# Kernel tuning notes

Measured on AMD Instinct MI355X. Metric: run time of the kernel, lower is better.

## Reference

```python
import jax, jax.numpy as jnp
from jax import lax
import numpy as np

COST_CLASS = 1.0
COST_BEZIER = 5.0
INF = jnp.float32(1e30)


def setup_inputs() -> dict:
    key = jax.random.key(0)
    k1, k2, k3, k4 = jax.random.split(key, 4)
    B, N, M, C = 16, 256, 256, 4096
    return {
        'pred_ctrl': jax.random.normal(k1, (B, N, 4, 2), dtype=jnp.float32),
        'pred_logits': jax.random.normal(k2, (B, N, C), dtype=jnp.float32),
        'gt_ctrl': jax.random.normal(k3, (B, M, 4, 2), dtype=jnp.float32),
        'gt_labels': jax.random.randint(k4, (B, M), 0, C, dtype=jnp.int64),
    }


def build_cost(pred_ctrl, pred_logits, gt_ctrl, gt_labels):
    B, N = pred_ctrl.shape[:2]
    M = gt_ctrl.shape[1]
    prob = jax.nn.softmax(pred_logits, axis=-1)                      # (B,N,C)
    lbl = jnp.broadcast_to(gt_labels[:, None, :], (B, N, M))          # (B,N,M)
    cost_class = -jnp.take_along_axis(prob, lbl, axis=2)              # (B,N,M)
    p = pred_ctrl.reshape(B, N, 8)
    g = gt_ctrl.reshape(B, M, 8)
    cost_bezier = jnp.sum(jnp.abs(p[:, :, None, :] - g[:, None, :, :]), axis=-1)  # L1 cdist
    return COST_CLASS * cost_class + COST_BEZIER * cost_bezier        # (B,N,M)


def lsa(cost):
    """Jonker-Volgenant shortest augmenting path, square n x n cost.
    Returns (row_ind, col_ind) matching scipy.optimize.linear_sum_assignment."""
    n = cost.shape[0]
    ar = jnp.arange(n)

    def solve_row(carry, cur_row):
        u, v, row4col, col4row = carry

        def cond(s):
            return s['sink'] < 0

        def body(s):
            i = s['i']
            SR = s['SR'].at[i].set(True)
            r = s['minVal'] + cost[i] - u[i] - v
            better = (r < s['spc']) & (~s['SC'])
            path = jnp.where(better, i, s['path'])
            spc = jnp.where(better, r, s['spc'])
            masked = jnp.where(s['SC'], INF, spc)
            j = jnp.argmin(masked).astype(jnp.int32)
            minVal = masked[j]
            SC = s['SC'].at[j].set(True)
            hit_free = row4col[j] < 0
            sink = jnp.where(hit_free, j, jnp.int32(-1))
            i_next = jnp.where(hit_free, i, row4col[j])
            return dict(i=i_next, minVal=minVal, SR=SR, SC=SC, spc=spc, path=path, sink=sink)

        init = dict(i=cur_row.astype(jnp.int32), minVal=jnp.float32(0),
                    SR=jnp.zeros(n, bool), SC=jnp.zeros(n, bool),
                    spc=jnp.full(n, INF), path=jnp.full(n, -1, jnp.int32),
                    sink=jnp.int32(-1))
        s = lax.while_loop(cond, body, init)
        minVal, SR, SC, spc, path, sink = s['minVal'], s['SR'], s['SC'], s['spc'], s['path'], s['sink']

        # dual updates
        u = u.at[cur_row].add(minVal)
        safe = jnp.clip(col4row, 0, n - 1)
        u = jnp.where(SR & (ar != cur_row), u + minVal - spc[safe], u)
        v = jnp.where(SC, v - (minVal - spc), v)

        # augment along predecessor path
        def aug_cond(t):
            return ~t['done']

        def aug_body(t):
            j = t['j']
            i = path[j]
            r4c = t['row4col'].at[j].set(i)
            j_next = t['col4row'][i]
            c4r = t['col4row'].at[i].set(j)
            return dict(j=j_next, row4col=r4c, col4row=c4r, done=(i == cur_row))

        t = lax.while_loop(aug_cond, aug_body,
                           dict(j=sink, row4col=row4col, col4row=col4row, done=jnp.bool_(False)))
        return (u, v, t['row4col'], t['col4row']), None

    init = (jnp.zeros(n, jnp.float32), jnp.zeros(n, jnp.float32),
            jnp.full(n, -1, jnp.int32), jnp.full(n, -1, jnp.int32))
    (u, v, row4col, col4row), _ = lax.scan(solve_row, init, ar)
    return ar.astype(jnp.int64), col4row.astype(jnp.int64)


_batched_lsa = jax.jit(jax.vmap(lsa))


def reference(pred_ctrl, pred_logits, gt_ctrl, gt_labels):
    C = build_cost(pred_ctrl, pred_logits, gt_ctrl, gt_labels)  # (B,N,M)
    row_ind, col_ind = _batched_lsa(C)                           # each (B,N)
    return row_ind, col_ind, C
```

## Files before the change

kernel.cpp:

```cpp
#include <hip/hip_runtime.h>

#define BATCH 16
#define NROW  256
#define MCOL  256
#define CDIM  4096
#define INF_F 1e30f
#define CROWS 150
#define MAXSWEEP 32
#define FREETHRESH 6

__global__ __launch_bounds__(256)
void cost_fused_kernel(const float* __restrict__ pred_ctrl,
                       const float* __restrict__ logits,
                       const float* __restrict__ gt_ctrl,
                       const int* __restrict__ gt_labels,
                       float* __restrict__ Cout) {
    const int bn = blockIdx.x;
    const int b  = bn >> 8;
    const int t  = threadIdx.x;
    const int lane = t & 63, wave = t >> 6;
    const float* rp = logits + (size_t)bn * CDIM;

    __shared__ float part[4];
    __shared__ float smax, ssum;

    float mx = -INF_F;
    for (int c = t; c < CDIM; c += 256) mx = fmaxf(mx, rp[c]);
    for (int off = 32; off; off >>= 1) mx = fmaxf(mx, __shfl_down(mx, off));
    if (lane == 0) part[wave] = mx;
    __syncthreads();
    if (t == 0) smax = fmaxf(fmaxf(part[0], part[1]), fmaxf(part[2], part[3]));
    __syncthreads();
    mx = smax;

    float s = 0.f;
    for (int c = t; c < CDIM; c += 256) s += expf(rp[c] - mx);
    for (int off = 32; off; off >>= 1) s += __shfl_down(s, off);
    __syncthreads();
    if (lane == 0) part[wave] = s;
    __syncthreads();
    if (t == 0) ssum = part[0] + part[1] + part[2] + part[3];
    __syncthreads();

    const float rmax = smax, rsum = ssum;
    const int m = t;

    const float* pp = pred_ctrl + (size_t)bn * 8;
    const float p0 = pp[0], p1 = pp[1], p2 = pp[2], p3 = pp[3];
    const float p4 = pp[4], p5 = pp[5], p6 = pp[6], p7 = pp[7];

    const float* gp = gt_ctrl + ((size_t)b * MCOL + m) * 8;
    const float4 ga = *(const float4*)gp;
    const float4 gb = *(const float4*)(gp + 4);

    const int lbl = gt_labels[b * MCOL + m];
    const float prob = expf(rp[lbl] - rmax) / rsum;

    float cb = fabsf(p0 - ga.x);
    cb += fabsf(p1 - ga.y);
    cb += fabsf(p2 - ga.z);
    cb += fabsf(p3 - ga.w);
    cb += fabsf(p4 - gb.x);
    cb += fabsf(p5 - gb.y);
    cb += fabsf(p6 - gb.z);
    cb += fabsf(p7 - gb.w);

    Cout[(size_t)bn * MCOL + m] = -prob + 5.0f * cb;
}

__device__ __forceinline__ unsigned ordkey(float f) {
    unsigned b = __float_as_uint(f);
    return (b & 0x80000000u) ? ~b : (b | 0x80000000u);
}
__device__ __forceinline__ float unordkey(unsigned k) {
    unsigned b = (k & 0x80000000u) ? (k ^ 0x80000000u) : ~k;
    return __uint_as_float(b);
}

template<int CTRL>
__device__ __forceinline__ unsigned dpp_min_step(unsigned x) {
    const unsigned o = (unsigned)__builtin_amdgcn_update_dpp((int)x, (int)x, CTRL, 0xf, 0xf, false);
    return o < x ? o : x;
}
__device__ __forceinline__ unsigned wave_min_u32(unsigned x) {
    x = dpp_min_step<0x111>(x);
    x = dpp_min_step<0x112>(x);
    x = dpp_min_step<0x114>(x);
    x = dpp_min_step<0x118>(x);
    x = dpp_min_step<0x142>(x);
    x = dpp_min_step<0x143>(x);
    return (unsigned)__builtin_amdgcn_readlane((int)x, 63);
}

__device__ __forceinline__ float readlane_f(float x, int lane_idx) {
    return __int_as_float(__builtin_amdgcn_readlane(__float_as_int(x), lane_idx));
}
__device__ __forceinline__ float sel4f(float a0, float a1, float a2, float a3, int s) {
    float r = a0;
    r = (s == 1) ? a1 : r;
    r = (s == 2) ? a2 : r;
    r = (s == 3) ? a3 : r;
    return r;
}
__device__ __forceinline__ int sel4i(int a0, int a1, int a2, int a3, int s) {
    int r = a0;
    r = (s == 1) ? a1 : r;
    r = (s == 2) ? a2 : r;
    r = (s == 3) ? a3 : r;
    return r;
}

__global__ __launch_bounds__(64)
void lsa_kernel(const float* __restrict__ Cmat,
                float* __restrict__ out_row,
                float* __restrict__ out_col) {
    const int b = blockIdx.x;
    const int t = threadIdx.x;
    const int jb = 4 * t;
    const float* C = Cmat + (size_t)b * NROW * MCOL;

    __shared__ float Cc[CROWS][MCOL];
    __shared__ __align__(16) float v_lds[MCOL];
    __shared__ unsigned long long bid_s[MCOL];
    __shared__ int r4c_s[MCOL];
    __shared__ int c4r_s[NROW];
    int* const argrow_s = (int*)bid_s;

    float m0 = INF_F, m1 = INF_F, m2 = INF_F, m3 = INF_F;
    int   r0 = 0, r1 = 0, r2 = 0, r3 = 0;
    for (int i = 0; i < NROW; i++) {
        const float4 c4 = *(const float4*)(C + (size_t)i * MCOL + jb);
        if (i < CROWS) *(float4*)&Cc[i][jb] = c4;
        if (c4.x < m0) { m0 = c4.x; r0 = i; }
        if (c4.y < m1) { m1 = c4.y; r1 = i; }
        if (c4.z < m2) { m2 = c4.z; r2 = i; }
        if (c4.w < m3) { m3 = c4.w; r3 = i; }
    }
    float u0 = 0.f, u1 = 0.f, u2 = 0.f, u3 = 0.f;

    v_lds[jb + 0] = m0; v_lds[jb + 1] = m1;
    v_lds[jb + 2] = m2; v_lds[jb + 3] = m3;
    argrow_s[jb + 0] = r0; argrow_s[jb + 1] = r1;
    argrow_s[jb + 2] = r2; argrow_s[jb + 3] = r3;
    for (int k = 0; k < 4; k++) { c4r_s[jb + k] = -1; r4c_s[jb + k] = -1; }
    __syncthreads();

    if (t == 0) {
        for (int j = 0; j < MCOL; j++) {
            const int r = argrow_s[j];
            if (c4r_s[r] < 0) { c4r_s[r] = j; r4c_s[j] = r; }
        }
    }
    __syncthreads();

    for (int sweep = 0; sweep < MAXSWEEP; sweep++) {
        const int4 myc = *(const int4*)&c4r_s[jb];
        const unsigned long long f0 = __ballot(myc.x < 0);
        const unsigned long long f1 = __ballot(myc.y < 0);
        const unsigned long long f2 = __ballot(myc.z < 0);
        const unsigned long long f3 = __ballot(myc.w < 0);
        const int nfree = __popcll(f0) + __popcll(f1) + __popcll(f2) + __popcll(f3);
        if (nfree <= FREETHRESH) break;

        bid_s[jb + 0] = 0; bid_s[jb + 1] = 0;
        bid_s[jb + 2] = 0; bid_s[jb + 3] = 0;
        __syncthreads();

        const bool fr[4] = { myc.x < 0, myc.y < 0, myc.z < 0, myc.w < 0 };
        int bj[4]; float gap[4], mu2v[4]; unsigned long long key[4];

        #pragma unroll
        for (int s = 0; s < 4; s++) {
            bj[s] = -1; gap[s] = 0.f; mu2v[s] = 0.f; key[s] = 0;
            if (!fr[s]) continue;
            const int i = jb + s;
            const float* rowp = C + (size_t)i * MCOL;
            unsigned bk1 = 0xFFFFFFFFu, bk2 = 0xFFFFFFFFu; int bjj = 0;
            for (int j = 0; j < MCOL; j += 4) {
                const float4 vv = *(const float4*)&v_lds[j];
                const float4 cc = *(const float4*)(rowp + j);
                unsigned k;
                k = ordkey(cc.x - vv.x); if (k < bk1) { bk2 = bk1; bk1 = k; bjj = j + 0; } else if (k < bk2) bk2 = k;
                k = ordkey(cc.y - vv.y); if (k < bk1) { bk2 = bk1; bk1 = k; bjj = j + 1; } else if (k < bk2) bk2 = k;
                k = ordkey(cc.z - vv.z); if (k < bk1) { bk2 = bk1; bk1 = k; bjj = j + 2; } else if (k < bk2) bk2 = k;
                k = ordkey(cc.w - vv.w); if (k < bk1) { bk2 = bk1; bk1 = k; bjj = j + 3; } else if (k < bk2) bk2 = k;
            }
            const float mu1 = unordkey(bk1), mu2 = unordkey(bk2);
            gap[s] = mu2 - mu1; mu2v[s] = mu2; bj[s] = bjj;
            key[s] = ((unsigned long long)ordkey(gap[s]) << 32) | (unsigned)i;
            atomicMax(&bid_s[bjj], key[s]);
        }
        __syncthreads();

        int kold[4];
        #pragma unroll
        for (int s = 0; s < 4; s++) {
            kold[s] = -2;
            if (bj[s] >= 0 && bid_s[bj[s]] == key[s]) kold[s] = r4c_s[bj[s]];
        }
        __syncthreads();

        #pragma unroll
        for (int s = 0; s < 4; s++) {
            if (kold[s] >= -1) {
                const int i = jb + s, j1 = bj[s];
                r4c_s[j1] = i;
                c4r_s[i] = j1;
                if (kold[s] >= 0) c4r_s[kold[s]] = -1;
                v_lds[j1] -= gap[s];
                if (s == 0) u0 = mu2v[0];
                else if (s == 1) u1 = mu2v[1];
                else if (s == 2) u2 = mu2v[2];
                else u3 = mu2v[3];
            }
        }
        __syncthreads();
    }

    int4 q;
    q = *(const int4*)&r4c_s[jb];
    int rc0 = q.x, rc1 = q.y, rc2 = q.z, rc3 = q.w;
    q = *(const int4*)&c4r_s[jb];
    int cr0 = q.x, cr1 = q.y, cr2 = q.z, cr3 = q.w;
    const float4 vq = *(const float4*)&v_lds[jb];
    float v0 = vq.x, v1 = vq.y, v2 = vq.z, v3 = vq.w;

    unsigned long long mm0 = __ballot(cr0 < 0);
    unsigned long long mm1 = __ballot(cr1 < 0);
    unsigned long long mm2 = __ballot(cr2 < 0);
    unsigned long long mm3 = __ballot(cr3 < 0);

    while (mm0 | mm1 | mm2 | mm3) {
        int cur;
        if      (mm0) { const int l = __ffsll(mm0) - 1; mm0 &= mm0 - 1; cur = 4 * l + 0; }
        else if (mm1) { const int l = __ffsll(mm1) - 1; mm1 &= mm1 - 1; cur = 4 * l + 1; }
        else if (mm2) { const int l = __ffsll(mm2) - 1; mm2 &= mm2 - 1; cur = 4 * l + 2; }
        else          { const int l = __ffsll(mm3) - 1; mm3 &= mm3 - 1; cur = 4 * l + 3; }

        float s0 = INF_F, s1 = INF_F, s2 = INF_F, s3 = INF_F;
        int   p0 = -1,    p1 = -1,    p2 = -1,    p3 = -1;
        float e0 = 0.f, e1 = 0.f, e2 = 0.f, e3 = 0.f;
        int scmask = 0, srmask = 0;
        int i = cur, sink = -1;
        float minVal = 0.f;

        for (int it = 0; it < MCOL; it++) {
            if ((i >> 2) == t) {
                const int s = i & 3;
                srmask |= 1 << s;
                e0 = s == 0 ? minVal : e0; e1 = s == 1 ? minVal : e1;
                e2 = s == 2 ? minVal : e2; e3 = s == 3 ? minVal : e3;
            }
            const float ui = readlane_f(sel4f(u0, u1, u2, u3, i & 3), i >> 2);
            float4 c4;
            if (i < CROWS) c4 = *(const float4*)&Cc[i][jb];
            else           c4 = *(const float4*)(C + (size_t)i * MCOL + jb);
            const float base = minVal - ui;
            float d;
            d = base + c4.x - v0; if (!(scmask & 1) && d < s0) { s0 = d; p0 = i; }
            d = base + c4.y - v1; if (!(scmask & 2) && d < s1) { s1 = d; p1 = i; }
            d = base + c4.z - v2; if (!(scmask & 4) && d < s2) { s2 = d; p2 = i; }
            d = base + c4.w - v3; if (!(scmask & 8) && d < s3) { s3 = d; p3 = i; }

            unsigned lmin = 0xFFFFFFFFu; int lslot = 0, lrc = -1;
            if (!(scmask & 1)) { const unsigned k = ordkey(s0); if (k < lmin) { lmin = k; lslot = 0; lrc = rc0; } }
            if (!(scmask & 2)) { const unsigned k = ordkey(s1); if (k < lmin) { lmin = k; lslot = 1; lrc = rc1; } }
            if (!(scmask & 4)) { const unsigned k = ordkey(s2); if (k < lmin) { lmin = k; lslot = 2; lrc = rc2; } }
            if (!(scmask & 8)) { const unsigned k = ordkey(s3); if (k < lmin) { lmin = k; lslot = 3; lrc = rc3; } }

            const unsigned g = wave_min_u32(lmin);
            const unsigned long long bal = __ballot(lmin == g);
            const int w = __ffsll(bal) - 1;
            const int pk = __builtin_amdgcn_readlane(((lrc + 1) << 2) | lslot, w);
            const int mj = 4 * w + (pk & 3);
            const int rcx = (pk >> 2) - 1;
            minVal = unordkey(g);

            if (w == t) scmask |= 1 << (pk & 3);
            if (rcx < 0) { sink = mj; break; }
            i = rcx;
        }

        if (srmask & 1) u0 += minVal - e0;
        if (srmask & 2) u1 += minVal - e1;
        if (srmask & 4) u2 += minVal - e2;
        if (srmask & 8) u3 += minVal - e3;
        if (scmask & 1) v0 -= (minVal - s0);
        if (scmask & 2) v1 -= (minVal - s1);
        if (scmask & 4) v2 -= (minVal - s2);
        if (scmask & 8) v3 -= (minVal - s3);

        int j = sink;
        for (int g2 = 0; g2 < NROW; g2++) {
            const int pi = __builtin_amdgcn_readlane(
                sel4i(p0, p1, p2, p3, j & 3), j >> 2);
            if ((j >> 2) == t) {
                const int s = j & 3;
                rc0 = s == 0 ? pi : rc0; rc1 = s == 1 ? pi : rc1;
                rc2 = s == 2 ? pi : rc2; rc3 = s == 3 ? pi : rc3;
            }
            const int jn = __builtin_amdgcn_readlane(
                sel4i(cr0, cr1, cr2, cr3, pi & 3), pi >> 2);
            if ((pi >> 2) == t) {
                const int s = pi & 3;
                cr0 = s == 0 ? j : cr0; cr1 = s == 1 ? j : cr1;
                cr2 = s == 2 ? j : cr2; cr3 = s == 3 ? j : cr3;
            }
            if (jn < 0) break;
            j = jn;
        }
    }

    out_row[b * NROW + jb + 0] = (float)(jb + 0);
    out_row[b * NROW + jb + 1] = (float)(jb + 1);
    out_row[b * NROW + jb + 2] = (float)(jb + 2);
    out_row[b * NROW + jb + 3] = (float)(jb + 3);
    out_col[b * NROW + jb + 0] = (float)cr0;
    out_col[b * NROW + jb + 1] = (float)cr1;
    out_col[b * NROW + jb + 2] = (float)cr2;
    out_col[b * NROW + jb + 3] = (float)cr3;
}

extern "C" void kernel_launch(void* const* d_in, const int* in_sizes, int n_in,
                              void* d_out, int out_size, void* d_ws, size_t ws_size,
                              hipStream_t stream) {
    const float* pred_ctrl   = (const float*)d_in[0];
    const float* pred_logits = (const float*)d_in[1];
    const float* gt_ctrl     = (const float*)d_in[2];
    const int*   gt_labels   = (const int*)d_in[3];

    float* out     = (float*)d_out;
    float* out_row = out;
    float* out_col = out + BATCH * NROW;
    float* Cout    = out + 2 * BATCH * NROW;

    cost_fused_kernel<<<BATCH * NROW, 256, 0, stream>>>(pred_ctrl, pred_logits,
                                                        gt_ctrl, gt_labels, Cout);
    lsa_kernel<<<BATCH, 64, 0, stream>>>(Cout, out_row, out_col);
}
```

Before: 1.784 ms.

## Replace greedy init and auction sweeps with epsilon-scaled auction warm start

Drops the column-min greedy initial assignment and the gap-based sweep loop that stopped at a small free-row threshold. In their place it runs an epsilon-scaling auction: four eps levels, the assignment is reset at each level, with per-level and total sweep caps. Afterwards it recomputes row duals as reduced-cost minima and unassigns any rows whose current match is not tight, so the exact augmenting-path phase starts from feasible duals. The aim is fewer rows left for the serial shortest-path augmentation. The risk is more auction sweeps, and possibly more rows unassigned by the tightness check.

```diff
diff --git a/kernel.cpp b/kernel.cpp
--- a/kernel.cpp
+++ b/kernel.cpp
@@ -6,8 +6,9 @@
 #define CDIM  4096
 #define INF_F 1e30f
 #define CROWS 150
-#define MAXSWEEP 32
-#define FREETHRESH 6
+#define NSCALE 4
+#define SWEEPCAP 40
+#define TOTBUDGET 120
 
 __global__ __launch_bounds__(256)
 void cost_fused_kernel(const float* __restrict__ pred_ctrl,
@@ -124,98 +125,113 @@
     __shared__ unsigned long long bid_s[MCOL];
     __shared__ int r4c_s[MCOL];
     __shared__ int c4r_s[NROW];
-    int* const argrow_s = (int*)bid_s;
 
     float m0 = INF_F, m1 = INF_F, m2 = INF_F, m3 = INF_F;
-    int   r0 = 0, r1 = 0, r2 = 0, r3 = 0;
     for (int i = 0; i < NROW; i++) {
         const float4 c4 = *(const float4*)(C + (size_t)i * MCOL + jb);
         if (i < CROWS) *(float4*)&Cc[i][jb] = c4;
-        if (c4.x < m0) { m0 = c4.x; r0 = i; }
-        if (c4.y < m1) { m1 = c4.y; r1 = i; }
-        if (c4.z < m2) { m2 = c4.z; r2 = i; }
-        if (c4.w < m3) { m3 = c4.w; r3 = i; }
+        m0 = fminf(m0, c4.x); m1 = fminf(m1, c4.y);
+        m2 = fminf(m2, c4.z); m3 = fminf(m3, c4.w);
     }
     float u0 = 0.f, u1 = 0.f, u2 = 0.f, u3 = 0.f;
 
     v_lds[jb + 0] = m0; v_lds[jb + 1] = m1;
     v_lds[jb + 2] = m2; v_lds[jb + 3] = m3;
-    argrow_s[jb + 0] = r0; argrow_s[jb + 1] = r1;
-    argrow_s[jb + 2] = r2; argrow_s[jb + 3] = r3;
-    for (int k = 0; k < 4; k++) { c4r_s[jb + k] = -1; r4c_s[jb + k] = -1; }
-    __syncthreads();
-
-    if (t == 0) {
-        for (int j = 0; j < MCOL; j++) {
-            const int r = argrow_s[j];
-            if (c4r_s[r] < 0) { c4r_s[r] = j; r4c_s[j] = r; }
+    __syncthreads();
+
+    const float eps_sched[NSCALE] = {1.0f, 0.1f, 0.01f, 0.001f};
+    int budget = TOTBUDGET;
+    for (int scale = 0; scale < NSCALE; scale++) {
+        const float eps = eps_sched[scale];
+        *(int4*)&c4r_s[jb] = make_int4(-1, -1, -1, -1);
+        *(int4*)&r4c_s[jb] = make_int4(-1, -1, -1, -1);
+        __syncthreads();
+
+        for (int sweep = 0; sweep < SWEEPCAP && budget > 0; sweep++, budget--) {
+            const int4 myc = *(const int4*)&c4r_s[jb];
+            const unsigned long long f0 = __ballot(myc.x < 0);
+            const unsigned long long f1 = __ballot(myc.y < 0);
+            const unsigned long long f2 = __ballot(myc.z < 0);
+            const unsigned long long f3 = __ballot(myc.w < 0);
+            if (!(f0 | f1 | f2 | f3)) break;
+
+            bid_s[jb + 0] = 0; bid_s[jb + 1] = 0;
+            bid_s[jb + 2] = 0; bid_s[jb + 3] = 0;
+            __syncthreads();
+
+            const bool fr[4] = { myc.x < 0, myc.y < 0, myc.z < 0, myc.w < 0 };
+            int bj[4]; float bump[4]; unsigned long long key[4];
+
+            #pragma unroll
+            for (int s = 0; s < 4; s++) {
+                bj[s] = -1; bump[s] = 0.f; key[s] = 0;
+                if (!fr[s]) continue;
+                const int i = jb + s;
+                const float* rowp = C + (size_t)i * MCOL;
+                float b1 = INF_F, b2 = INF_F; int idx = 0;
+                for (int j = 0; j < MCOL; j += 4) {
+                    const float4 vv = *(const float4*)&v_lds[j];
+                    const float4 cc = *(const float4*)(rowp + j);
+                    float d;
+                    d = cc.x - vv.x; b2 = fminf(b2, fmaxf(b1, d)); idx = d < b1 ? j + 0 : idx; b1 = fminf(b1, d);
+                    d = cc.y - vv.y; b2 = fminf(b2, fmaxf(b1, d)); idx = d < b1 ? j + 1 : idx; b1 = fminf(b1, d);
+                    d = cc.z - vv.z; b2 = fminf(b2, fmaxf(b1, d)); idx = d < b1 ? j + 2 : idx; b1 = fminf(b1, d);
+                    d = cc.w - vv.w; b2 = fminf(b2, fmaxf(b1, d)); idx = d < b1 ? j + 3 : idx; b1 = fminf(b1, d);
+                }
+                bump[s] = (b2 - b1) + eps;
+                bj[s] = idx;
+                key[s] = ((unsigned long long)ordkey(bump[s]) << 32) | (unsigned)i;
+                atomicMax(&bid_s[idx], key[s]);
+            }
+            __syncthreads();
+
+            int kold[4];
+            #pragma unroll
+            for (int s = 0; s < 4; s++) {
+                kold[s] = -2;
+                if (bj[s] >= 0 && bid_s[bj[s]] == key[s]) kold[s] = r4c_s[bj[s]];
+            }
+            __syncthreads();
+
+            #pragma unroll
+            for (int s = 0; s < 4; s++) {
+                if (kold[s] >= -1) {
+                    const int i = jb + s, j1 = bj[s];
+                    r4c_s[j1] = i;
+                    c4r_s[i] = j1;
+                    if (kold[s] >= 0) c4r_s[kold[s]] = -1;
+                    v_lds[j1] -= bump[s];
+                }
+            }
+            __syncthreads();
         }
     }
-    __syncthreads();
-
-    for (int sweep = 0; sweep < MAXSWEEP; sweep++) {
-        const int4 myc = *(const int4*)&c4r_s[jb];
-        const unsigned long long f0 = __ballot(myc.x < 0);
-        const unsigned long long f1 = __ballot(myc.y < 0);
-        const unsigned long long f2 = __ballot(myc.z < 0);
-        const unsigned long long f3 = __ballot(myc.w < 0);
-        const int nfree = __popcll(f0) + __popcll(f1) + __popcll(f2) + __popcll(f3);
-        if (nfree <= FREETHRESH) break;
-
-        bid_s[jb + 0] = 0; bid_s[jb + 1] = 0;
-        bid_s[jb + 2] = 0; bid_s[jb + 3] = 0;
-        __syncthreads();
-
-        const bool fr[4] = { myc.x < 0, myc.y < 0, myc.z < 0, myc.w < 0 };
-        int bj[4]; float gap[4], mu2v[4]; unsigned long long key[4];
-
+
+    {
+        float uu[4];
         #pragma unroll
         for (int s = 0; s < 4; s++) {
-            bj[s] = -1; gap[s] = 0.f; mu2v[s] = 0.f; key[s] = 0;
-            if (!fr[s]) continue;
             const int i = jb + s;
             const float* rowp = C + (size_t)i * MCOL;
-            unsigned bk1 = 0xFFFFFFFFu, bk2 = 0xFFFFFFFFu; int bjj = 0;
+            float b1 = INF_F;
             for (int j = 0; j < MCOL; j += 4) {
                 const float4 vv = *(const float4*)&v_lds[j];
                 const float4 cc = *(const float4*)(rowp + j);
-                unsigned k;
-                k = ordkey(cc.x - vv.x); if (k < bk1) { bk2 = bk1; bk1 = k; bjj = j + 0; } else if (k < bk2) bk2 = k;
-                k = ordkey(cc.y - vv.y); if (k < bk1) { bk2 = bk1; bk1 = k; bjj = j + 1; } else if (k < bk2) bk2 = k;
-                k = ordkey(cc.z - vv.z); if (k < bk1) { bk2 = bk1; bk1 = k; bjj = j + 2; } else if (k < bk2) bk2 = k;
-                k = ordkey(cc.w - vv.w); if (k < bk1) { bk2 = bk1; bk1 = k; bjj = j + 3; } else if (k < bk2) bk2 = k;
-            }
-            const float mu1 = unordkey(bk1), mu2 = unordkey(bk2);
-            gap[s] = mu2 - mu1; mu2v[s] = mu2; bj[s] = bjj;
-            key[s] = ((unsigned long long)ordkey(gap[s]) << 32) | (unsigned)i;
-            atomicMax(&bid_s[bjj], key[s]);
+                b1 = fminf(b1, cc.x - vv.x);
+                b1 = fminf(b1, cc.y - vv.y);
+                b1 = fminf(b1, cc.z - vv.z);
+                b1 = fminf(b1, cc.w - vv.w);
+            }
+            uu[s] = b1;
+            const int jm = c4r_s[i];
+            if (jm >= 0) {
+                const float rm = rowp[jm] - v_lds[jm];
+                if (rm > b1) { c4r_s[i] = -1; r4c_s[jm] = -1; }
+            }
         }
-        __syncthreads();
-
-        int kold[4];
-        #pragma unroll
-        for (int s = 0; s < 4; s++) {
-            kold[s] = -2;
-            if (bj[s] >= 0 && bid_s[bj[s]] == key[s]) kold[s] = r4c_s[bj[s]];
-        }
-        __syncthreads();
-
-        #pragma unroll
-        for (int s = 0; s < 4; s++) {
-            if (kold[s] >= -1) {
-                const int i = jb + s, j1 = bj[s];
-                r4c_s[j1] = i;
-                c4r_s[i] = j1;
-                if (kold[s] >= 0) c4r_s[kold[s]] = -1;
-                v_lds[j1] -= gap[s];
-                if (s == 0) u0 = mu2v[0];
-                else if (s == 1) u1 = mu2v[1];
-                else if (s == 2) u2 = mu2v[2];
-                else u3 = mu2v[3];
-            }
-        }
-        __syncthreads();
+        u0 = uu[0]; u1 = uu[1]; u2 = uu[2]; u3 = uu[3];
     }
+    __syncthreads();
 
     int4 q;
     q = *(const int4*)&r4c_s[jb];
```

New measurement: 2.756 ms. 1.54x slower.
